# Kernel tuning notes

Measured on AMD Instinct MI355X. Metric: run time of the kernel, lower is better.

The kernel has to match this reference:

```python
import jax, jax.numpy as jnp
import numpy as np

L, B, D, H = 256, 128, 512, 512


def setup_inputs() -> dict:
    key = jax.random.key(0)
    ks = jax.random.split(key, 16)
    sx = 1.0 / np.sqrt(D)
    sh = 1.0 / np.sqrt(H)
    inp = {
        "inputs": jax.random.normal(ks[0], (L, B, D), jnp.float32),
        "Wi_x": jax.random.normal(ks[1], (H, D), jnp.float32) * sx,
        "bi_x": jax.random.normal(ks[2], (H,), jnp.float32) * sx,
        "Wi_h": jax.random.normal(ks[3], (H, H), jnp.float32) * sh,
        "bi_h": jax.random.normal(ks[4], (H,), jnp.float32) * sh,
        "Wf_x": jax.random.normal(ks[5], (H, D), jnp.float32) * sx,
        "bf_x": jax.random.normal(ks[6], (H,), jnp.float32) * sx,
        "Wf_h": jax.random.normal(ks[7], (H, H), jnp.float32) * sh,
        "bf_h": jax.random.normal(ks[8], (H,), jnp.float32) * sh,
        "Wo_x": jax.random.normal(ks[9], (H, D), jnp.float32) * sx,
        "Wo_h": jax.random.normal(ks[10], (H, H), jnp.float32) * sh,
        "Wu_x": jax.random.normal(ks[11], (H, D), jnp.float32) * sx,
        "Wu_h": jax.random.normal(ks[12], (H, H), jnp.float32) * sh,
    }
    # Random tree topology: node t's parent is a random earlier node (topological order),
    # node 0 is the root (parent = -1 -> zero parent state).
    rng = np.random.default_rng(0)
    parents = np.full((L, B), -1, dtype=np.int32)
    for t in range(1, L):
        parents[t] = rng.integers(0, t, size=B)
    inp["parents"] = jnp.asarray(parents)
    return inp


def reference(inputs, Wi_x, bi_x, Wi_h, bi_h, Wf_x, bf_x, Wf_h, bf_h,
              Wo_x, Wo_h, Wu_x, Wu_h, parents):
    Lm, Bm, _ = inputs.shape
    Hd = Wi_h.shape[0]
    batch_ar = jnp.arange(Bm)

    def step(carry, xs):
        Hbuf, Cbuf = carry  # [B, L, H] each
        x, p, t = xs        # x: [B, D], p: [B] parent node index (-1 = root), t: scalar
        valid = (p >= 0)[:, None]
        pi = jnp.maximum(p, 0)
        ph = jnp.where(valid, Hbuf[batch_ar, pi], 0.0)
        pc = jnp.where(valid, Cbuf[batch_ar, pi], 0.0)
        i = jax.nn.sigmoid(x @ Wi_x.T + bi_x + ph @ Wi_h.T + bi_h)
        f = jax.nn.sigmoid(x @ Wf_x.T + bf_x + ph @ Wf_h.T + bf_h)
        o = jax.nn.sigmoid(x @ Wo_x.T + ph @ Wo_h.T)
        u = jnp.tanh(x @ Wu_x.T + ph @ Wu_h.T)
        c = i * u + f * pc
        h = o * jnp.tanh(c)
        Hbuf = Hbuf.at[:, t].set(h)
        Cbuf = Cbuf.at[:, t].set(c)
        return (Hbuf, Cbuf), None

    init = (jnp.zeros((Bm, Lm, Hd), inputs.dtype),
            jnp.zeros((Bm, Lm, Hd), inputs.dtype))
    (Hbuf, _), _ = jax.lax.scan(step, init, (inputs, parents, jnp.arange(Lm)))
    return Hbuf  # [B, L, H], matching torch output layout
```

## Files before the change

kernel.cpp:

```cpp
#include <hip/hip_runtime.h>
#include <hip/hip_bf16.h>

static constexpr int LL = 256;
static constexpr int BB = 128;
static constexpr int HHH = 512;

typedef __attribute__((ext_vector_type(8))) short bf16x8;
typedef __attribute__((ext_vector_type(4))) float f32x4;
typedef __attribute__((ext_vector_type(8))) unsigned short u16x8;
typedef __attribute__((ext_vector_type(4))) unsigned short u16x4;

__device__ __forceinline__ unsigned short f2bf(float f) {
  union { float f; unsigned u; } v; v.f = f;
  unsigned r = (v.u + 0x7FFFu + ((v.u >> 16) & 1u)) >> 16;
  return (unsigned short)r;
}
__device__ __forceinline__ float bf2f(unsigned short s) {
  union { unsigned u; float f; } v; v.u = ((unsigned)s) << 16;
  return v.f;
}
__device__ __forceinline__ float sigm(float x) { return 1.0f / (1.0f + __expf(-x)); }
__device__ __forceinline__ float tanh_f(float x) { return 1.0f - 2.0f / (__expf(2.0f * x) + 1.0f); }

__global__ __launch_bounds__(256) void prep(
    const float* __restrict__ s0, const float* __restrict__ s1,
    const float* __restrict__ s2, const float* __restrict__ s3,
    const float* __restrict__ h0, const float* __restrict__ h1,
    const float* __restrict__ h2, const float* __restrict__ h3,
    const int* __restrict__ parents,
    unsigned short* __restrict__ wx, unsigned short* __restrict__ whp,
    int* __restrict__ pairs, int* __restrict__ lmeta, int* __restrict__ mrows,
    int* __restrict__ flag) {
  const int blk = blockIdx.x;
  const int tid = threadIdx.x;
  if (blk < 1024) {
    int gid = blk * 256 + tid;
    int e = gid * 4;
    int m = e >> 18;
    int off = e & 0x3FFFF;
    const float* srcs[4] = {s0, s1, s2, s3};
    float4 v = *(const float4*)(srcs[m] + off);
    u16x4 o;
    o[0] = f2bf(v.x); o[1] = f2bf(v.y); o[2] = f2bf(v.z); o[3] = f2bf(v.w);
    *(u16x4*)(wx + (size_t)m * 262144 + off) = o;
  } else if (blk < 1536) {
    int gid = (blk - 1024) * 256 + tid;
    int lane = gid & 63;
    int kb   = (gid >> 6) & 15;
    int n16  = (gid >> 10) & 31;
    int g    = gid >> 15;
    const float* W = (g == 0) ? h0 : (g == 1) ? h1 : (g == 2) ? h2 : h3;
    int row = n16 * 16 + (lane & 15);
    int col = kb * 32 + (lane >> 4) * 8;
    const float4* s = (const float4*)(W + (size_t)row * 512 + col);
    float4 v0 = s[0], v1 = s[1];
    u16x8 o;
    o[0] = f2bf(v0.x); o[1] = f2bf(v0.y); o[2] = f2bf(v0.z); o[3] = f2bf(v0.w);
    o[4] = f2bf(v1.x); o[5] = f2bf(v1.y); o[6] = f2bf(v1.z); o[7] = f2bf(v1.w);
    *(u16x8*)&whp[(size_t)gid * 8] = o;
  } else if (blk == 1536) {
    __shared__ unsigned short cnt2[128][130];
    __shared__ int off[130];
    __shared__ int maxl_sh;
    const int b = tid;
    unsigned char mylvl[256];
    if (b < 128) {
      for (int l = 0; l < 130; ++l) cnt2[b][l] = 0;
    }
    if (b == 0) maxl_sh = 0;
    __syncthreads();
    if (b < 128) {
      int maxl = 0;
      for (int t = 0; t < 256; ++t) {
        int p = parents[t * 128 + b];
        int l = (p < 0) ? 0 : (mylvl[p] + 1);
        if (l > 127) l = 127;
        mylvl[t] = (unsigned char)l;
        maxl = l > maxl ? l : maxl;
        cnt2[b][l]++;
      }
      atomicMax(&maxl_sh, maxl);
    }
    __syncthreads();
    const int nlev = maxl_sh + 1;
    if (b < 128) {
      int l = b;
      int s = 0;
      if (l < nlev) for (int bb = 0; bb < 128; ++bb) s += cnt2[bb][l];
      off[l + 1] = s;
    }
    __syncthreads();
    if (b == 0) {
      off[0] = 0;
      for (int l = 0; l < 128; ++l) off[l + 1] += off[l];
    }
    __syncthreads();
    if (b < 128) {
      int l = b;
      if (l < nlev) {
        int run = off[l];
        for (int bb = 0; bb < 128; ++bb) {
          int c = cnt2[bb][l];
          cnt2[bb][l] = (unsigned short)run;
          run += c;
        }
      }
    }
    __syncthreads();
    if (b < 128) {
      for (int t = 0; t < 256; ++t) {
        int l = mylvl[t];
        int pos = cnt2[b][l]++;
        pairs[pos] = t * 128 + b;
      }
    }
    if (b == 0) {
      int midx = 0;
      for (int l = 0; l < nlev; ++l) {
        int s = off[l], e = off[l + 1];
        for (int rb = s; rb < e; rb += 32) {
          int rc = (e - rb < 32) ? (e - rb) : 32;
          mrows[midx++] = (rb << 6) | rc;
        }
      }
      lmeta[0] = midx;
    }
  } else {
    int i = (blk - 1537) * 256 + tid;
    if (i < LL * BB) flag[i] = 0;
  }
}

__global__ __launch_bounds__(256) void xproj3(
    const float* __restrict__ X, const unsigned short* __restrict__ Wx,
    const float* __restrict__ bi_x, const float* __restrict__ bi_h,
    const float* __restrict__ bf_x, const float* __restrict__ bf_h,
    unsigned short* __restrict__ Xpre) {
  __shared__ unsigned short As[128 * 64];
  __shared__ unsigned short Bs[128 * 64];
  const int m0 = blockIdx.x * 128;
  const int n0 = blockIdx.y * 128;
  const int tid = threadIdx.x;
  const int lane = tid & 63, w = tid >> 6;
  const int wr = w >> 1, wc = w & 1;
  const int hi = lane >> 4, l15 = lane & 15;
  f32x4 acc[4][4] = {};
  for (int kt = 0; kt < 8; ++kt) {
    const int k0 = kt * 64;
    __syncthreads();
#pragma unroll
    for (int i = 0; i < 4; ++i) {
      const int grp = i * 4 + w;
      const int unit = grp * 64 + lane;
      const int row = unit >> 3, c8p = unit & 7;
      const int c8l = c8p ^ (row & 7);
      const unsigned short* gb = Wx + (size_t)(n0 + row) * 512 + k0 + c8l * 8;
      __builtin_amdgcn_global_load_lds(
          (const __attribute__((address_space(1))) unsigned int*)gb,
          (__attribute__((address_space(3))) unsigned int*)(Bs + grp * 512),
          16, 0, 0);
    }
#pragma unroll
    for (int i = 0; i < 4; ++i) {
      const int unit = i * 256 + tid;
      const int row = unit >> 3, c8l = unit & 7;
      const float* src = X + (size_t)(m0 + row) * 512 + k0 + c8l * 8;
      float4 v0 = ((const float4*)src)[0];
      float4 v1 = ((const float4*)src)[1];
      u16x8 o;
      o[0] = f2bf(v0.x); o[1] = f2bf(v0.y); o[2] = f2bf(v0.z); o[3] = f2bf(v0.w);
      o[4] = f2bf(v1.x); o[5] = f2bf(v1.y); o[6] = f2bf(v1.z); o[7] = f2bf(v1.w);
      *(u16x8*)&As[row * 64 + ((c8l ^ (row & 7)) << 3)] = o;
    }
    __syncthreads();
#pragma unroll
    for (int kk = 0; kk < 2; ++kk) {
      const int kofs = kk * 32 + hi * 8;
      bf16x8 a[4], bb[4];
#pragma unroll
      for (int mi = 0; mi < 4; ++mi) {
        const int row = wr * 64 + mi * 16 + l15;
        a[mi] = *(const bf16x8*)&As[row * 64 + (kofs ^ ((row & 7) << 3))];
      }
#pragma unroll
      for (int ni = 0; ni < 4; ++ni) {
        const int row = wc * 64 + ni * 16 + l15;
        bb[ni] = *(const bf16x8*)&Bs[row * 64 + (kofs ^ ((row & 7) << 3))];
      }
#pragma unroll
      for (int mi = 0; mi < 4; ++mi)
#pragma unroll
        for (int ni = 0; ni < 4; ++ni)
          acc[mi][ni] = __builtin_amdgcn_mfma_f32_16x16x32_bf16(a[mi], bb[ni], acc[mi][ni], 0, 0, 0);
    }
  }
#pragma unroll
  for (int ni = 0; ni < 4; ++ni) {
    const int col = n0 + wc * 64 + ni * 16 + l15;
    const int g = col >> 9, hh = col & 511;
    float badd = 0.0f;
    if (g == 0) badd = bi_x[hh] + bi_h[hh];
    else if (g == 1) badd = bf_x[hh] + bf_h[hh];
#pragma unroll
    for (int mi = 0; mi < 4; ++mi) {
      const int rbase = m0 + wr * 64 + mi * 16 + hi * 4;
#pragma unroll
      for (int q = 0; q < 4; ++q)
        Xpre[(size_t)(rbase + q) * 2048 + col] = f2bf(acc[mi][ni][q] + badd);
    }
  }
}

__global__ __launch_bounds__(512, 2) void treelstm_static(
    const unsigned short* __restrict__ Xpre,
    const unsigned short* __restrict__ Whp,
    const int* __restrict__ parents,
    const int* __restrict__ pairs,
    const int* __restrict__ lmeta,
    const int* __restrict__ mrows,
    int* __restrict__ flag,
    float* __restrict__ Hout,
    float* __restrict__ Cbuf,
    unsigned short* __restrict__ Hbf) {
  __shared__ unsigned short phs[32][536];
  __shared__ float gbuf[4][32][66];
  const int tid = threadIdx.x;
  const int lane = tid & 63, w = tid >> 6;
  const int g = w & 3, nh = w >> 2;
  const int ct = blockIdx.x & 7;
  const int slot = blockIdx.x >> 3;
  const int mcnt = lmeta[0];
  const int hi = lane >> 4, l15 = lane & 15;

  bf16x8 wfrag[2][16];
  {
    const size_t base = (size_t)((g * 32 + ct * 4 + nh * 2) * 16) * 512 + lane * 8;
#pragma unroll
    for (int kb = 0; kb < 16; ++kb) {
      wfrag[0][kb] = *(const bf16x8*)&Whp[base + (size_t)kb * 512];
      wfrag[1][kb] = *(const bf16x8*)&Whp[base + (size_t)(16 + kb) * 512];
    }
  }
#pragma unroll
  for (int kb = 0; kb < 16; ++kb) {
    asm volatile("" : "+v"(wfrag[0][kb]));
    asm volatile("" : "+v"(wfrag[1][kb]));
  }

  for (int my = slot; my < mcnt; my += 32) {
    const int mr = mrows[my];
    const int rbase = mr >> 6;
    const int rcnt = mr & 63;

    const int r = tid >> 4;
    const int q16 = tid & 15;
    const int hc = q16 * 4;
    const int h = ct * 64 + hc;
    int node = 0, p = -1, b = 0;
    if (r < rcnt) {
      node = pairs[rbase + r];
      p = parents[node];
      b = node & 127;
    }
    u16x4 xga[4] = {};
    if (r < rcnt) {
#pragma unroll
      for (int gg = 0; gg < 4; ++gg)
        xga[gg] = *(const u16x4*)(Xpre + (size_t)node * 2048 + gg * 512 + h);
    }

    if (tid < 32) {
      int pn = -1;
      if (tid < rcnt) {
        const int node2 = pairs[rbase + tid];
        const int p2 = parents[node2];
        if (p2 >= 0) pn = p2 * 128 + (node2 & 127);
      }
      if (pn >= 0) {
        while (__hip_atomic_load(&flag[pn], __ATOMIC_RELAXED,
                                 __HIP_MEMORY_SCOPE_AGENT) < 8)
          __builtin_amdgcn_s_sleep(1);
      }
    }
    __syncthreads();

    float4 pc = make_float4(0.f, 0.f, 0.f, 0.f);
    if (r < rcnt && p >= 0)
      pc = *(const float4*)(Cbuf + ((size_t)b * LL + p) * HHH + h);
    if (p >= 0) {
      const unsigned short* src = Hbf + ((size_t)b * LL + p) * HHH + q16 * 32;
#pragma unroll
      for (int j = 0; j < 4; ++j)
        *(u16x8*)&phs[r][q16 * 32 + j * 8] = ((const u16x8*)src)[j];
    } else {
      u16x8 z = {};
#pragma unroll
      for (int j = 0; j < 4; ++j) *(u16x8*)&phs[r][q16 * 32 + j * 8] = z;
    }
    __syncthreads();

    f32x4 acc[2][2] = {};
#pragma unroll
    for (int kb = 0; kb < 16; ++kb) {
      const int ko = kb * 32 + 8 * hi;
      bf16x8 a0 = *(const bf16x8*)&phs[l15][ko];
      bf16x8 a1 = *(const bf16x8*)&phs[16 + l15][ko];
      acc[0][0] = __builtin_amdgcn_mfma_f32_16x16x32_bf16(a0, wfrag[0][kb], acc[0][0], 0, 0, 0);
      acc[1][0] = __builtin_amdgcn_mfma_f32_16x16x32_bf16(a1, wfrag[0][kb], acc[1][0], 0, 0, 0);
      acc[0][1] = __builtin_amdgcn_mfma_f32_16x16x32_bf16(a0, wfrag[1][kb], acc[0][1], 0, 0, 0);
      acc[1][1] = __builtin_amdgcn_mfma_f32_16x16x32_bf16(a1, wfrag[1][kb], acc[1][1], 0, 0, 0);
    }
#pragma unroll
    for (int mi = 0; mi < 2; ++mi)
#pragma unroll
      for (int ni = 0; ni < 2; ++ni)
#pragma unroll
        for (int qq = 0; qq < 4; ++qq)
          gbuf[g][mi * 16 + hi * 4 + qq][nh * 32 + ni * 16 + l15] = acc[mi][ni][qq];
    __syncthreads();

    float hva[4];
    size_t obase = 0;
    if (r < rcnt) {
      const int t = node >> 7;
      float xg[4][4];
#pragma unroll
      for (int gg = 0; gg < 4; ++gg)
#pragma unroll
        for (int j = 0; j < 4; ++j) xg[gg][j] = bf2f(xga[gg][j]);
      const float pcv[4] = {pc.x, pc.y, pc.z, pc.w};
      float cva[4];
#pragma unroll
      for (int j = 0; j < 4; ++j) {
        float iv = sigm(gbuf[0][r][hc + j] + xg[0][j]);
        float fv = sigm(gbuf[1][r][hc + j] + xg[1][j]);
        float ov = sigm(gbuf[2][r][hc + j] + xg[2][j]);
        float uv = tanh_f(gbuf[3][r][hc + j] + xg[3][j]);
        float cv = iv * uv + fv * pcv[j];
        cva[j] = cv;
        hva[j] = ov * tanh_f(cv);
      }
      obase = ((size_t)b * LL + t) * HHH + h;
      union { float f[4]; unsigned long long u[2]; } cvu;
      cvu.f[0] = cva[0]; cvu.f[1] = cva[1]; cvu.f[2] = cva[2]; cvu.f[3] = cva[3];
      unsigned long long* cp = (unsigned long long*)(Cbuf + obase);
      __hip_atomic_store(cp, cvu.u[0], __ATOMIC_RELAXED, __HIP_MEMORY_SCOPE_AGENT);
      __hip_atomic_store(cp + 1, cvu.u[1], __ATOMIC_RELAXED, __HIP_MEMORY_SCOPE_AGENT);
      union { unsigned short s[4]; unsigned long long u; } hbu;
      hbu.s[0] = f2bf(hva[0]); hbu.s[1] = f2bf(hva[1]);
      hbu.s[2] = f2bf(hva[2]); hbu.s[3] = f2bf(hva[3]);
      __hip_atomic_store((unsigned long long*)(Hbf + obase), hbu.u,
                         __ATOMIC_RELAXED, __HIP_MEMORY_SCOPE_AGENT);
    }
    asm volatile("s_waitcnt vmcnt(0)" ::: "memory");
    if (r < rcnt && q16 == 0)
      __hip_atomic_fetch_add(&flag[node], 1, __ATOMIC_RELAXED,
                             __HIP_MEMORY_SCOPE_AGENT);
    if (r < rcnt)
      *(float4*)(Hout + obase) = make_float4(hva[0], hva[1], hva[2], hva[3]);
    __syncthreads();
  }
}

extern "C" void kernel_launch(void* const* d_in, const int* in_sizes, int n_in,
                              void* d_out, int out_size, void* d_ws, size_t ws_size,
                              hipStream_t stream) {
  const float* X    = (const float*)d_in[0];
  const float* Wi_x = (const float*)d_in[1];
  const float* bi_x = (const float*)d_in[2];
  const float* Wi_h = (const float*)d_in[3];
  const float* bi_h = (const float*)d_in[4];
  const float* Wf_x = (const float*)d_in[5];
  const float* bf_x = (const float*)d_in[6];
  const float* Wf_h = (const float*)d_in[7];
  const float* bf_h = (const float*)d_in[8];
  const float* Wo_x = (const float*)d_in[9];
  const float* Wo_h = (const float*)d_in[10];
  const float* Wu_x = (const float*)d_in[11];
  const float* Wu_h = (const float*)d_in[12];
  const int* parents = (const int*)d_in[13];
  float* Hout = (float*)d_out;

  char* ws = (char*)d_ws;
  unsigned short* Xpre = (unsigned short*)ws; ws += (size_t)32768 * 2048 * 2;
  unsigned short* Hbf  = (unsigned short*)ws; ws += (size_t)BB * LL * HHH * 2;
  float*          Cbuf = (float*)ws;          ws += (size_t)BB * LL * HHH * 4;
  unsigned short* Wxbf = (unsigned short*)ws; ws += (size_t)2048 * 512 * 2;
  unsigned short* Whp  = (unsigned short*)ws; ws += (size_t)2048 * 512 * 2;
  int*            pairs = (int*)ws;           ws += (size_t)32768 * 4;
  int*            lmeta = (int*)ws;           ws += 256 * 4;
  int*            mrows = (int*)ws;           ws += 4096 * 4;
  int*            flag  = (int*)ws;           ws += (size_t)32768 * 4;

  prep<<<1665, 256, 0, stream>>>(Wi_x, Wf_x, Wo_x, Wu_x,
                                 Wi_h, Wf_h, Wo_h, Wu_h,
                                 parents, Wxbf, Whp, pairs, lmeta, mrows, flag);
  dim3 g1(256, 16);
  xproj3<<<g1, 256, 0, stream>>>(X, Wxbf, bi_x, bi_h, bf_x, bf_h, Xpre);

  treelstm_static<<<256, 512, 0, stream>>>(Xpre, Whp, parents, pairs, lmeta,
                                           mrows, flag, Hout, Cbuf, Hbf);
}
```

Before: 610.8 us.

## Use atomic ticket work distribution, more resident blocks, bf16 gate buffer, staged xproj stores

The recurrent tree-LSTM kernel stops assigning row-chunks round-robin by static slot. Blocks now grab chunks through a per-column-tile atomic ticket counter, and twice as many blocks are launched with a higher occupancy bound. The gate accumulator buffer in shared memory shrinks to bf16 so more blocks can fit per CU, at the cost of extra rounding on the gate pre-activations. The x-projection GEMM epilogue stages its output through LDS so global stores are coalesced 16-byte writes instead of scattered 2-byte ones. The dynamic ticket order together with the flag-based dependency waiting could add contention or spinning.

```diff
diff --git a/kernel.cpp b/kernel.cpp
--- a/kernel.cpp
+++ b/kernel.cpp
@@ -30,7 +30,7 @@
     const int* __restrict__ parents,
     unsigned short* __restrict__ wx, unsigned short* __restrict__ whp,
     int* __restrict__ pairs, int* __restrict__ lmeta, int* __restrict__ mrows,
-    int* __restrict__ flag) {
+    int* __restrict__ flag, int* __restrict__ tick) {
   const int blk = blockIdx.x;
   const int tid = threadIdx.x;
   if (blk < 1024) {
@@ -128,6 +128,7 @@
   } else {
     int i = (blk - 1537) * 256 + tid;
     if (i < LL * BB) flag[i] = 0;
+    if (blk == 1537 && tid < 8) tick[tid] = 0;
   }
 }
 
@@ -136,8 +137,7 @@
     const float* __restrict__ bi_x, const float* __restrict__ bi_h,
     const float* __restrict__ bf_x, const float* __restrict__ bf_h,
     unsigned short* __restrict__ Xpre) {
-  __shared__ unsigned short As[128 * 64];
-  __shared__ unsigned short Bs[128 * 64];
+  __shared__ unsigned short Sh[2][8192];
   const int m0 = blockIdx.x * 128;
   const int n0 = blockIdx.y * 128;
   const int tid = threadIdx.x;
@@ -157,7 +157,7 @@
       const unsigned short* gb = Wx + (size_t)(n0 + row) * 512 + k0 + c8l * 8;
       __builtin_amdgcn_global_load_lds(
           (const __attribute__((address_space(1))) unsigned int*)gb,
-          (__attribute__((address_space(3))) unsigned int*)(Bs + grp * 512),
+          (__attribute__((address_space(3))) unsigned int*)(&Sh[1][grp * 512]),
           16, 0, 0);
     }
 #pragma unroll
@@ -170,7 +170,7 @@
       u16x8 o;
       o[0] = f2bf(v0.x); o[1] = f2bf(v0.y); o[2] = f2bf(v0.z); o[3] = f2bf(v0.w);
       o[4] = f2bf(v1.x); o[5] = f2bf(v1.y); o[6] = f2bf(v1.z); o[7] = f2bf(v1.w);
-      *(u16x8*)&As[row * 64 + ((c8l ^ (row & 7)) << 3)] = o;
+      *(u16x8*)&Sh[0][row * 64 + ((c8l ^ (row & 7)) << 3)] = o;
     }
     __syncthreads();
 #pragma unroll
@@ -180,12 +180,12 @@
 #pragma unroll
       for (int mi = 0; mi < 4; ++mi) {
         const int row = wr * 64 + mi * 16 + l15;
-        a[mi] = *(const bf16x8*)&As[row * 64 + (kofs ^ ((row & 7) << 3))];
+        a[mi] = *(const bf16x8*)&Sh[0][row * 64 + (kofs ^ ((row & 7) << 3))];
       }
 #pragma unroll
       for (int ni = 0; ni < 4; ++ni) {
         const int row = wc * 64 + ni * 16 + l15;
-        bb[ni] = *(const bf16x8*)&Bs[row * 64 + (kofs ^ ((row & 7) << 3))];
+        bb[ni] = *(const bf16x8*)&Sh[1][row * 64 + (kofs ^ ((row & 7) << 3))];
       }
 #pragma unroll
       for (int mi = 0; mi < 4; ++mi)
@@ -194,24 +194,35 @@
           acc[mi][ni] = __builtin_amdgcn_mfma_f32_16x16x32_bf16(a[mi], bb[ni], acc[mi][ni], 0, 0, 0);
     }
   }
+  __syncthreads();
+  unsigned short* Cs = &Sh[0][0];
 #pragma unroll
   for (int ni = 0; ni < 4; ++ni) {
-    const int col = n0 + wc * 64 + ni * 16 + l15;
-    const int g = col >> 9, hh = col & 511;
+    const int coll = wc * 64 + ni * 16 + l15;
+    const int gcol = n0 + coll;
+    const int g = gcol >> 9, hh = gcol & 511;
     float badd = 0.0f;
     if (g == 0) badd = bi_x[hh] + bi_h[hh];
     else if (g == 1) badd = bf_x[hh] + bf_h[hh];
 #pragma unroll
     for (int mi = 0; mi < 4; ++mi) {
-      const int rbase = m0 + wr * 64 + mi * 16 + hi * 4;
+      const int rbase = wr * 64 + mi * 16 + hi * 4;
 #pragma unroll
       for (int q = 0; q < 4; ++q)
-        Xpre[(size_t)(rbase + q) * 2048 + col] = f2bf(acc[mi][ni][q] + badd);
-    }
-  }
-}
-
-__global__ __launch_bounds__(512, 2) void treelstm_static(
+        Cs[(rbase + q) * 128 + coll] = f2bf(acc[mi][ni][q] + badd);
+    }
+  }
+  __syncthreads();
+#pragma unroll
+  for (int u = 0; u < 8; ++u) {
+    const int unit = u * 256 + tid;
+    const int row = unit >> 4, c8 = unit & 15;
+    *(u16x8*)&Xpre[(size_t)(m0 + row) * 2048 + n0 + c8 * 8] =
+        *(const u16x8*)&Cs[row * 128 + c8 * 8];
+  }
+}
+
+__global__ __launch_bounds__(512, 4) void treelstm_flag(
     const unsigned short* __restrict__ Xpre,
     const unsigned short* __restrict__ Whp,
     const int* __restrict__ parents,
@@ -219,16 +230,17 @@
     const int* __restrict__ lmeta,
     const int* __restrict__ mrows,
     int* __restrict__ flag,
+    int* __restrict__ tick,
     float* __restrict__ Hout,
     float* __restrict__ Cbuf,
     unsigned short* __restrict__ Hbf) {
   __shared__ unsigned short phs[32][536];
-  __shared__ float gbuf[4][32][66];
+  __shared__ unsigned short gbuf[4][32][66];
+  __shared__ int sh_ticket;
   const int tid = threadIdx.x;
   const int lane = tid & 63, w = tid >> 6;
   const int g = w & 3, nh = w >> 2;
   const int ct = blockIdx.x & 7;
-  const int slot = blockIdx.x >> 3;
   const int mcnt = lmeta[0];
   const int hi = lane >> 4, l15 = lane & 15;
 
@@ -247,7 +259,12 @@
     asm volatile("" : "+v"(wfrag[1][kb]));
   }
 
-  for (int my = slot; my < mcnt; my += 32) {
+  while (true) {
+    __syncthreads();
+    if (tid == 0) sh_ticket = atomicAdd(&tick[ct], 1);
+    __syncthreads();
+    const int my = sh_ticket;
+    if (my >= mcnt) break;
     const int mr = mrows[my];
     const int rbase = mr >> 6;
     const int rcnt = mr & 63;
@@ -316,12 +333,14 @@
       for (int ni = 0; ni < 2; ++ni)
 #pragma unroll
         for (int qq = 0; qq < 4; ++qq)
-          gbuf[g][mi * 16 + hi * 4 + qq][nh * 32 + ni * 16 + l15] = acc[mi][ni][qq];
+          gbuf[g][mi * 16 + hi * 4 + qq][nh * 32 + ni * 16 + l15] =
+              f2bf(acc[mi][ni][qq]);
     __syncthreads();
 
     float hva[4];
     size_t obase = 0;
-    if (r < rcnt) {
+    bool valid = (r < rcnt);
+    if (valid) {
       const int t = node >> 7;
       float xg[4][4];
 #pragma unroll
@@ -332,10 +351,10 @@
       float cva[4];
 #pragma unroll
       for (int j = 0; j < 4; ++j) {
-        float iv = sigm(gbuf[0][r][hc + j] + xg[0][j]);
-        float fv = sigm(gbuf[1][r][hc + j] + xg[1][j]);
-        float ov = sigm(gbuf[2][r][hc + j] + xg[2][j]);
-        float uv = tanh_f(gbuf[3][r][hc + j] + xg[3][j]);
+        float iv = sigm(bf2f(gbuf[0][r][hc + j]) + xg[0][j]);
+        float fv = sigm(bf2f(gbuf[1][r][hc + j]) + xg[1][j]);
+        float ov = sigm(bf2f(gbuf[2][r][hc + j]) + xg[2][j]);
+        float uv = tanh_f(bf2f(gbuf[3][r][hc + j]) + xg[3][j]);
         float cv = iv * uv + fv * pcv[j];
         cva[j] = cv;
         hva[j] = ov * tanh_f(cv);
@@ -353,12 +372,11 @@
                          __ATOMIC_RELAXED, __HIP_MEMORY_SCOPE_AGENT);
     }
     asm volatile("s_waitcnt vmcnt(0)" ::: "memory");
-    if (r < rcnt && q16 == 0)
+    if (valid && q16 == 0)
       __hip_atomic_fetch_add(&flag[node], 1, __ATOMIC_RELAXED,
                              __HIP_MEMORY_SCOPE_AGENT);
-    if (r < rcnt)
+    if (valid)
       *(float4*)(Hout + obase) = make_float4(hva[0], hva[1], hva[2], hva[3]);
-    __syncthreads();
   }
 }
 
@@ -391,13 +409,15 @@
   int*            lmeta = (int*)ws;           ws += 256 * 4;
   int*            mrows = (int*)ws;           ws += 4096 * 4;
   int*            flag  = (int*)ws;           ws += (size_t)32768 * 4;
+  int*            tick  = (int*)ws;           ws += 64 * 4;
 
   prep<<<1665, 256, 0, stream>>>(Wi_x, Wf_x, Wo_x, Wu_x,
                                  Wi_h, Wf_h, Wo_h, Wu_h,
-                                 parents, Wxbf, Whp, pairs, lmeta, mrows, flag);
+                                 parents, Wxbf, Whp, pairs, lmeta, mrows,
+                                 flag, tick);
   dim3 g1(256, 16);
   xproj3<<<g1, 256, 0, stream>>>(X, Wxbf, bi_x, bi_h, bf_x, bf_h, Xpre);
 
-  treelstm_static<<<256, 512, 0, stream>>>(Xpre, Whp, parents, pairs, lmeta,
-                                           mrows, flag, Hout, Cbuf, Hbf);
-}
+  treelstm_flag<<<512, 512, 0, stream>>>(Xpre, Whp, parents, pairs, lmeta,
+                                         mrows, flag, tick, Hout, Cbuf, Hbf);
+}
```

After: 701.7 us. 14.9% more time.
